# Performance work log

Hardware: AMD Instinct MI355X
Metric: run time of the kernel (lower is better)

The kernel has to match this reference:

```python
import jax, jax.numpy as jnp
import numpy as np

WINDOW_LENGTH = 8  # hop size used by overlap_and_add (matches init_kwargs)


def overlap_and_add(x, step):
    """x: [B, C, T, L] frames; returns [B, C, (T-1)*step + L].
    Requires L % step == 0 (standard Conv-TasNet overlap_and_add)."""
    B, C, T, L = x.shape
    k = L // step  # subframes per frame
    sub = x.reshape(B, C, T * k, step)
    # subframe j of frame t lands at output subframe t + j
    seg = (jnp.arange(T)[:, None] + jnp.arange(k)[None, :]).reshape(-1)
    out = jnp.zeros((B, C, T + k - 1, step), x.dtype).at[:, :, seg].add(sub)
    return out.reshape(B, C, (T + k - 1) * step)


def setup_inputs() -> dict:
    key = jax.random.key(0)
    k1, k2 = jax.random.split(key)
    B, C, D, T = 8, 2, 16, 128000
    x = jax.random.normal(k1, (B, C, D, T), dtype=jnp.float32)
    x_wave = jax.random.normal(k2, (B, D, T), dtype=jnp.float32)
    return {"x": x, "x_wave": x_wave, "pad_left": 8, "pad_right": 8}


def reference(x, x_wave, pad_left, pad_right):
    # x: [B, C, D, T] masks; x_wave: [B, D, T] encoder output
    x = x * x_wave[:, None]              # broadcast over speaker axis C
    x = jnp.transpose(x, (0, 1, 3, 2))   # [B, C, T, D] -> frames of length D
    y = overlap_and_add(x, WINDOW_LENGTH)  # [B, C, (T-1)*hop + D]
    if pad_right:
        y = y[:, :, pad_left:y.shape[-1] - pad_right]
    else:
        y = y[:, :, pad_left:]
    return y
```

## Files before the change

### kernel.cpp

```cpp
#include <hip/hip_runtime.h>


constexpr int B = 8;
constexpr int C = 2;
constexpr int D = 16;
constexpr int T = 128000;

constexpr int SEGS  = 256;
constexpr int PITCH = 260;
constexpr int NBLK  = T / SEGS;

__global__ __launch_bounds__(256, 4) void oaa_lds_kernel(
    const float* __restrict__ x,
    const float* __restrict__ xw,
    float* __restrict__ out,
    int S)
{
    __shared__ float P[C][D][PITCH];

    const int j  = threadIdx.x;
    const int b  = blockIdx.y;
    const int s0 = blockIdx.x * SEGS;

    const float* __restrict__ xwb = xw + (size_t)b * D * T;
    const float* __restrict__ xb0 = x  + (size_t)b * C * D * T;
    const float* __restrict__ xb1 = xb0 + (size_t)D * T;

#pragma unroll
    for (int i = 0; i < 4; ++i) {
        const int tau = j + 256 * i;
        const int d   = tau >> 6;
        const int col = tau & 63;
        const size_t g = (size_t)d * T + (size_t)(s0 + 4 * col);
        const float4 wv  = *(const float4*)(xwb + g);
        const float4 xv0 = *(const float4*)(xb0 + g);
        const float4 xv1 = *(const float4*)(xb1 + g);
        *(float4*)&P[0][d][4 + 4 * col] =
            make_float4(xv0.x * wv.x, xv0.y * wv.y, xv0.z * wv.z, xv0.w * wv.w);
        *(float4*)&P[1][d][4 + 4 * col] =
            make_float4(xv1.x * wv.x, xv1.y * wv.y, xv1.z * wv.z, xv1.w * wv.w);
    }
    if (j < 8) {
        const int d  = j + 8;
        const int th = (s0 >= 4) ? (s0 - 4) : 0;
        const size_t g = (size_t)d * T + (size_t)th;
        const float4 wv  = *(const float4*)(xwb + g);
        const float4 xv0 = *(const float4*)(xb0 + g);
        const float4 xv1 = *(const float4*)(xb1 + g);
        *(float4*)&P[0][d][0] =
            make_float4(xv0.x * wv.x, xv0.y * wv.y, xv0.z * wv.z, xv0.w * wv.w);
        *(float4*)&P[1][d][0] =
            make_float4(xv1.x * wv.x, xv1.y * wv.y, xv1.z * wv.z, xv1.w * wv.w);
    }
    __syncthreads();

    const size_t ob = (size_t)b * C * S;
#pragma unroll
    for (int i = 0; i < 4; ++i) {
        const int sig  = j + 256 * i;
        const int half = sig & 1;
        const int sloc = (sig >> 1) & (SEGS - 1);
        const int c    = sig >> 9;
        const int seg  = s0 + sloc;
        if (seg != 0) {
            const int dbase = 4 * half;
            const int ta = sloc + 4;
            const int tb = sloc + 3;
            float4 o;
            o.x = P[c][dbase + 0][ta] + P[c][dbase +  8][tb];
            o.y = P[c][dbase + 1][ta] + P[c][dbase +  9][tb];
            o.z = P[c][dbase + 2][ta] + P[c][dbase + 10][tb];
            o.w = P[c][dbase + 3][ta] + P[c][dbase + 11][tb];
            *(float4*)(out + ob + (size_t)c * S + (size_t)seg * 8 - 8 + dbase) = o;
        }
    }
}

extern "C" void kernel_launch(void* const* d_in, const int* in_sizes, int n_in,
                              void* d_out, int out_size, void* d_ws, size_t ws_size,
                              hipStream_t stream) {
    const float* x  = (const float*)d_in[0];
    const float* xw = (const float*)d_in[1];
    float* out = (float*)d_out;

    const int S = out_size / (B * C);
    dim3 grid(NBLK, B);
    oaa_lds_kernel<<<grid, dim3(256), 0, stream>>>(x, xw, out, S);
}
```

Measured before the change: 251.3 us.

## Process longer segments per block and reuse encoder weights across both speakers

Each block now covers 1024 segments instead of 256, holds the x_wave tile in registers, and handles the two speakers one after the other through a single-channel LDS buffer. The second speaker's mask loads are issued before the first speaker's output pass, so their latency can overlap that pass. The halo now loads only the one needed element per row. In exchange register pressure rises sharply (W and X1 arrays, launch bounds reduced to 2 waves per SIMD), there are fewer blocks, and an extra barrier is added between the speaker passes.

Measured after the change: 255.9 us. Within noise of the previous version (+1.8%).

```diff
diff --git a/kernel.cpp b/kernel.cpp
--- a/kernel.cpp
+++ b/kernel.cpp
@@ -6,72 +6,122 @@
 constexpr int D = 16;
 constexpr int T = 128000;
 
-constexpr int SEGS  = 256;
-constexpr int PITCH = 260;
+constexpr int SEGS  = 1024;
+constexpr int PITCH = 1028;
 constexpr int NBLK  = T / SEGS;
 
-__global__ __launch_bounds__(256, 4) void oaa_lds_kernel(
+__global__ __launch_bounds__(256, 2) void oaa_longrun_kernel(
     const float* __restrict__ x,
     const float* __restrict__ xw,
     float* __restrict__ out,
     int S)
 {
-    __shared__ float P[C][D][PITCH];
+    __shared__ float P[D][PITCH];
 
-    const int j  = threadIdx.x;
-    const int b  = blockIdx.y;
-    const int s0 = blockIdx.x * SEGS;
+    const int j    = threadIdx.x;
+    const int lane = j & 63;
+    const int wv   = j >> 6;
+    const int b    = blockIdx.y;
+    const int s0   = blockIdx.x * SEGS;
 
     const float* __restrict__ xwb = xw + (size_t)b * D * T;
     const float* __restrict__ xb0 = x  + (size_t)b * C * D * T;
     const float* __restrict__ xb1 = xb0 + (size_t)D * T;
 
+    float4 W[4][4];
+    float4 X1[4][4];
+    float  wh = 0.f, xh1 = 0.f;
+
 #pragma unroll
-    for (int i = 0; i < 4; ++i) {
-        const int tau = j + 256 * i;
-        const int d   = tau >> 6;
-        const int col = tau & 63;
-        const size_t g = (size_t)d * T + (size_t)(s0 + 4 * col);
-        const float4 wv  = *(const float4*)(xwb + g);
-        const float4 xv0 = *(const float4*)(xb0 + g);
-        const float4 xv1 = *(const float4*)(xb1 + g);
-        *(float4*)&P[0][d][4 + 4 * col] =
-            make_float4(xv0.x * wv.x, xv0.y * wv.y, xv0.z * wv.z, xv0.w * wv.w);
-        *(float4*)&P[1][d][4 + 4 * col] =
-            make_float4(xv1.x * wv.x, xv1.y * wv.y, xv1.z * wv.z, xv1.w * wv.w);
+    for (int r = 0; r < 4; ++r) {
+        const int d = 4 * wv + r;
+        const float* wp = xwb + (size_t)d * T + s0 + 4 * lane;
+        const float* xp = xb0 + (size_t)d * T + s0 + 4 * lane;
+        float4 X0[4];
+#pragma unroll
+        for (int q = 0; q < 4; ++q) W[r][q] = *(const float4*)(wp + 256 * q);
+#pragma unroll
+        for (int q = 0; q < 4; ++q) X0[q]   = *(const float4*)(xp + 256 * q);
+#pragma unroll
+        for (int q = 0; q < 4; ++q) {
+            float4 pr;
+            pr.x = W[r][q].x * X0[q].x;
+            pr.y = W[r][q].y * X0[q].y;
+            pr.z = W[r][q].z * X0[q].z;
+            pr.w = W[r][q].w * X0[q].w;
+            *(float4*)&P[d][4 + 256 * q + 4 * lane] = pr;
+        }
     }
     if (j < 8) {
-        const int d  = j + 8;
-        const int th = (s0 >= 4) ? (s0 - 4) : 0;
-        const size_t g = (size_t)d * T + (size_t)th;
-        const float4 wv  = *(const float4*)(xwb + g);
-        const float4 xv0 = *(const float4*)(xb0 + g);
-        const float4 xv1 = *(const float4*)(xb1 + g);
-        *(float4*)&P[0][d][0] =
-            make_float4(xv0.x * wv.x, xv0.y * wv.y, xv0.z * wv.z, xv0.w * wv.w);
-        *(float4*)&P[1][d][0] =
-            make_float4(xv1.x * wv.x, xv1.y * wv.y, xv1.z * wv.z, xv1.w * wv.w);
+        const int dh = 8 + j;
+        const size_t th = (s0 > 0) ? (size_t)(s0 - 1) : 0;
+        wh  = xwb[(size_t)dh * T + th];
+        const float xh0 = xb0[(size_t)dh * T + th];
+        xh1 = xb1[(size_t)dh * T + th];
+        P[dh][3] = wh * xh0;
+    }
+#pragma unroll
+    for (int r = 0; r < 4; ++r) {
+        const int d = 4 * wv + r;
+        const float* xp = xb1 + (size_t)d * T + s0 + 4 * lane;
+#pragma unroll
+        for (int q = 0; q < 4; ++q) X1[r][q] = *(const float4*)(xp + 256 * q);
     }
     __syncthreads();
 
     const size_t ob = (size_t)b * C * S;
 #pragma unroll
-    for (int i = 0; i < 4; ++i) {
+    for (int i = 0; i < 8; ++i) {
         const int sig  = j + 256 * i;
         const int half = sig & 1;
-        const int sloc = (sig >> 1) & (SEGS - 1);
-        const int c    = sig >> 9;
+        const int sloc = sig >> 1;
         const int seg  = s0 + sloc;
         if (seg != 0) {
             const int dbase = 4 * half;
             const int ta = sloc + 4;
             const int tb = sloc + 3;
             float4 o;
-            o.x = P[c][dbase + 0][ta] + P[c][dbase +  8][tb];
-            o.y = P[c][dbase + 1][ta] + P[c][dbase +  9][tb];
-            o.z = P[c][dbase + 2][ta] + P[c][dbase + 10][tb];
-            o.w = P[c][dbase + 3][ta] + P[c][dbase + 11][tb];
-            *(float4*)(out + ob + (size_t)c * S + (size_t)seg * 8 - 8 + dbase) = o;
+            o.x = P[dbase + 0][ta] + P[dbase +  8][tb];
+            o.y = P[dbase + 1][ta] + P[dbase +  9][tb];
+            o.z = P[dbase + 2][ta] + P[dbase + 10][tb];
+            o.w = P[dbase + 3][ta] + P[dbase + 11][tb];
+            *(float4*)(out + ob + (size_t)seg * 8 - 8 + dbase) = o;
+        }
+    }
+    __syncthreads();
+
+#pragma unroll
+    for (int r = 0; r < 4; ++r) {
+        const int d = 4 * wv + r;
+#pragma unroll
+        for (int q = 0; q < 4; ++q) {
+            float4 pr;
+            pr.x = W[r][q].x * X1[r][q].x;
+            pr.y = W[r][q].y * X1[r][q].y;
+            pr.z = W[r][q].z * X1[r][q].z;
+            pr.w = W[r][q].w * X1[r][q].w;
+            *(float4*)&P[d][4 + 256 * q + 4 * lane] = pr;
+        }
+    }
+    if (j < 8) P[8 + j][3] = wh * xh1;
+    __syncthreads();
+
+#pragma unroll
+    for (int i = 0; i < 8; ++i) {
+        const int sig  = j + 256 * i;
+        const int half = sig & 1;
+        const int sloc = sig >> 1;
+        const int seg  = s0 + sloc;
+        if (seg != 0) {
+            const int dbase = 4 * half;
+            const int ta = sloc + 4;
+            const int tb = sloc + 3;
+            float4 o;
+            o.x = P[dbase + 0][ta] + P[dbase +  8][tb];
+            o.y = P[dbase + 1][ta] + P[dbase +  9][tb];
+            o.z = P[dbase + 2][ta] + P[dbase + 10][tb];
+            o.w = P[dbase + 3][ta] + P[dbase + 11][tb];
+            *(float4*)(out + ob + (size_t)S + (size_t)seg * 8 - 8 + dbase) = o;
         }
     }
 }
@@ -85,5 +135,5 @@
 
     const int S = out_size / (B * C);
     dim3 grid(NBLK, B);
-    oaa_lds_kernel<<<grid, dim3(256), 0, stream>>>(x, xw, out, S);
+    oaa_longrun_kernel<<<grid, dim3(256), 0, stream>>>(x, xw, out, S);
 }
```
